# Kernel tuning notes

Measured on AMD Instinct MI355X. Metric: run time of the kernel, lower is better.

The kernel has to match this reference:

```python
import jax, jax.numpy as jnp
import numpy as np

DIM = 384
HEADS = 6
HEAD_DIM = DIM // HEADS
HIDDEN = int(DIM * 4.0)
LS_INIT = 1e-5
EPS = 1e-5


def _ln(x, w, b):
    mu = jnp.mean(x, axis=-1, keepdims=True)
    var = jnp.var(x, axis=-1, keepdims=True)
    return (x - mu) * jax.lax.rsqrt(var + EPS) * w + b


def setup_inputs() -> dict:
    key = jax.random.key(0)
    ks = jax.random.split(key, 12)
    s = 0.02
    eye = jnp.eye(HIDDEN, dtype=jnp.float32)
    return {
        "x": jax.random.normal(ks[0], (8, 2048, DIM), dtype=jnp.float32),
        "qkv_w": jax.random.normal(ks[1], (3 * DIM, DIM), dtype=jnp.float32) * s,
        "qkv_b": jnp.zeros((3 * DIM,), dtype=jnp.float32),
        "proj_w": jax.random.normal(ks[2], (DIM, DIM), dtype=jnp.float32) * s,
        "proj_b": jnp.zeros((DIM,), dtype=jnp.float32),
        "fc1_w": jax.random.normal(ks[3], (HIDDEN, DIM), dtype=jnp.float32) * s,
        "fc1_b": jnp.zeros((HIDDEN,), dtype=jnp.float32),
        "eye1_w": eye + jax.random.normal(ks[4], (HIDDEN, HIDDEN), dtype=jnp.float32) * s,
        "eye2_w": eye + jax.random.normal(ks[5], (HIDDEN, HIDDEN), dtype=jnp.float32) * s,
        "fc2_w": jax.random.normal(ks[6], (DIM, HIDDEN), dtype=jnp.float32) * s,
        "fc2_b": jnp.zeros((DIM,), dtype=jnp.float32),
        "norm1_w": jnp.ones((DIM,), dtype=jnp.float32),
        "norm1_b": jnp.zeros((DIM,), dtype=jnp.float32),
        "norm2_w": jnp.ones((DIM,), dtype=jnp.float32),
        "norm2_b": jnp.zeros((DIM,), dtype=jnp.float32),
        "ls1_gamma": jnp.full((DIM,), LS_INIT, dtype=jnp.float32),
        "ls2_gamma": jnp.full((DIM,), LS_INIT, dtype=jnp.float32),
    }


def reference(x, qkv_w, qkv_b, proj_w, proj_b, fc1_w, fc1_b, eye1_w, eye2_w,
              fc2_w, fc2_b, norm1_w, norm1_b, norm2_w, norm2_b, ls1_gamma, ls2_gamma):
    B, N, C = x.shape
    scale = HEAD_DIM ** -0.5

    # ---- attention branch ----
    h = _ln(x, norm1_w, norm1_b)
    qkv = h @ qkv_w.T + qkv_b                      # [B,N,3C]
    qkv = qkv.reshape(B, N, 3, HEADS, HEAD_DIM)
    q = qkv[:, :, 0].transpose(0, 2, 1, 3) * scale  # [B,H,N,D]
    k = qkv[:, :, 1].transpose(0, 2, 1, 3)
    v = qkv[:, :, 2].transpose(0, 2, 1, 3)
    attn = jax.nn.softmax(jnp.einsum('bhnd,bhmd->bhnm', q, k), axis=-1)  # [B,H,N,N]
    o = jnp.einsum('bhnm,bhmd->bhnd', attn, v)
    o = o.transpose(0, 2, 1, 3).reshape(B, N, C)
    o = o @ proj_w.T + proj_b
    x = x + o * ls1_gamma

    # ---- extended MLP branch (timm Mlp norm is Identity) ----
    h2 = _ln(x, norm2_w, norm2_b)
    a = jax.nn.gelu(h2 @ fc1_w.T + fc1_b, approximate=False)
    a = (a @ eye1_w.T) @ eye2_w.T
    a = a @ fc2_w.T + fc2_b
    return x + a * ls2_gamma
```

## Files before the change

### kernel.cpp

```cpp
#include <hip/hip_runtime.h>
#include <math.h>

#define DIM 384
#define HEADS 6
#define HEAD_DIM 64
#define HIDDEN 1536
#define BATCH 8
#define SEQ 2048
#define TOKENS (BATCH * SEQ)

typedef __bf16 bf16;
typedef float f32x4 __attribute__((ext_vector_type(4)));
typedef float f32x16 __attribute__((ext_vector_type(16)));
typedef int i32x2 __attribute__((ext_vector_type(2)));
typedef int i32x4 __attribute__((ext_vector_type(4)));
typedef int i32x8 __attribute__((ext_vector_type(8)));

#define GLOAD_LDS(gp, lp)                                                      \
    __builtin_amdgcn_global_load_lds(                                          \
        (const __attribute__((address_space(1))) void*)(gp),                   \
        (__attribute__((address_space(3))) void*)(lp), 16, 0, 0)

__device__ __forceinline__ unsigned char to_fp8(float v) {
    return (unsigned char)(__builtin_amdgcn_cvt_pk_fp8_f32(v, v, 0, false) & 0xff);
}

__device__ __forceinline__ i32x8 pack8(i32x4 lo, i32x4 hi) {
    i32x8 r;
#pragma unroll
    for (int j = 0; j < 4; j++) { r[j] = lo[j]; r[4 + j] = hi[j]; }
    return r;
}

#define NW_QKV  (1152 * 384)
#define NW_PROJ (384 * 384)
#define NW_FC1  (1536 * 384)
#define NW_EYE  (1536 * 1536)
#define NW_FC2  (384 * 1536)
#define NW_ALL2 (NW_QKV + NW_PROJ + NW_FC1 + NW_EYE + NW_FC2)

__global__ void convert_w8(const float* __restrict__ qkv, const float* __restrict__ proj,
                           const float* __restrict__ fc1, const float* __restrict__ e2,
                           const float* __restrict__ fc2, unsigned char* __restrict__ dst) {
    int q4 = blockIdx.x * 256 + threadIdx.x;
    int stride = gridDim.x * 256;
    for (; q4 < NW_ALL2 / 4; q4 += stride) {
        int i = q4 * 4;
        int j = i;
        const float* src;
        if (j < NW_QKV) src = qkv;
        else if ((j -= NW_QKV) < NW_PROJ) src = proj;
        else if ((j -= NW_PROJ) < NW_FC1) src = fc1;
        else if ((j -= NW_FC1) < NW_EYE) src = e2;
        else { j -= NW_EYE; src = fc2; }
        float4 v = *(const float4*)(src + j);
        int p = __builtin_amdgcn_cvt_pk_fp8_f32(v.x, v.y, 0, false);
        p = __builtin_amdgcn_cvt_pk_fp8_f32(v.z, v.w, p, true);
        *(int*)(dst + i) = p;
    }
}

__global__ __launch_bounds__(256) void transpose_f8(const float* __restrict__ in,
                                                    unsigned char* __restrict__ outT) {
    __shared__ float t[64][65];
    int r0 = blockIdx.y * 64, c0 = blockIdx.x * 64;
    int tc = threadIdx.x & 63, tr = threadIdx.x >> 6;
#pragma unroll
    for (int i = 0; i < 16; i++) {
        int r = tr + 4 * i;
        t[r][tc] = in[(size_t)(r0 + r) * 1536 + c0 + tc];
    }
    __syncthreads();
    int on = threadIdx.x >> 2;
    int ok0 = (threadIdx.x & 3) * 16;
    i32x4 pk;
#pragma unroll
    for (int q = 0; q < 4; q++) {
        int p = __builtin_amdgcn_cvt_pk_fp8_f32(t[ok0 + 4 * q + 0][on],
                                                t[ok0 + 4 * q + 1][on], 0, false);
        p = __builtin_amdgcn_cvt_pk_fp8_f32(t[ok0 + 4 * q + 2][on],
                                            t[ok0 + 4 * q + 3][on], p, true);
        pk[q] = p;
    }
    *(i32x4*)(outT + (size_t)(c0 + on) * 1536 + r0 + ok0) = pk;
}

__global__ __launch_bounds__(256) void ln_kernel(const float* __restrict__ x,
                                                 const float* __restrict__ w,
                                                 const float* __restrict__ b,
                                                 unsigned char* __restrict__ out) {
    int wave = threadIdx.x >> 6;
    int lane = threadIdx.x & 63;
    int t = blockIdx.x * 4 + wave;
    const float* xr = x + (size_t)t * DIM;
    float v[6];
    float s = 0.f;
#pragma unroll
    for (int i = 0; i < 6; i++) { v[i] = xr[lane + 64 * i]; s += v[i]; }
#pragma unroll
    for (int m = 1; m < 64; m <<= 1) s += __shfl_xor(s, m, 64);
    float mu = s * (1.f / DIM);
    float q = 0.f;
#pragma unroll
    for (int i = 0; i < 6; i++) { float d = v[i] - mu; q += d * d; }
#pragma unroll
    for (int m = 1; m < 64; m <<= 1) q += __shfl_xor(q, m, 64);
    float rstd = rsqrtf(q * (1.f / DIM) + 1e-5f);
    unsigned char* orow = out + (size_t)t * DIM;
#pragma unroll
    for (int i = 0; i < 6; i++) {
        int c = lane + 64 * i;
        orow[c] = to_fp8((v[i] - mu) * rstd * w[c] + b[c]);
    }
}

template <int EPI>
__global__ __launch_bounds__(256) void gemm_f8(const unsigned char* __restrict__ A,
                                               const unsigned char* __restrict__ W,
                                               const float* __restrict__ bias,
                                               float* __restrict__ outf,
                                               const float* __restrict__ resid,
                                               const float* __restrict__ gamma,
                                               unsigned char* __restrict__ vtb8,
                                               unsigned char* __restrict__ out8,
                                               int N, int K) {
    __shared__ __attribute__((aligned(16))) unsigned char As[128 * 128];
    __shared__ __attribute__((aligned(16))) unsigned char Bs[128 * 128];
    int tid = threadIdx.x;
    int wave = tid >> 6, lane = tid & 63;
    int l15 = lane & 15, quad = lane >> 4;
    int bm = blockIdx.y * 128, bn = blockIdx.x * 128;
    int wm = (wave & 1) * 64, wn = (wave >> 1) * 64;
    f32x4 acc[4][4] = {};

    for (int k0 = 0; k0 < K; k0 += 128) {
#pragma unroll
        for (int i = 0; i < 4; i++) {
            int slot = i * 256 + tid;
            int rr = slot >> 3;
            int gg = (slot & 7) ^ (rr & 7);
            GLOAD_LDS(A + (size_t)(bm + rr) * K + k0 + gg * 16,
                      (char*)As + (i * 256 + wave * 64) * 16);
            GLOAD_LDS(W + (size_t)(bn + rr) * K + k0 + gg * 16,
                      (char*)Bs + (i * 256 + wave * 64) * 16);
        }
        __syncthreads();
        i32x8 af[4], bfr[4];
#pragma unroll
        for (int mt = 0; mt < 4; mt++) {
            int rA = wm + mt * 16 + l15;
            const i32x4* p = (const i32x4*)(As + 128 * rA);
            af[mt] = pack8(p[(2 * quad) ^ (rA & 7)], p[(2 * quad + 1) ^ (rA & 7)]);
        }
#pragma unroll
        for (int nt = 0; nt < 4; nt++) {
            int rB = wn + nt * 16 + l15;
            const i32x4* p = (const i32x4*)(Bs + 128 * rB);
            bfr[nt] = pack8(p[(2 * quad) ^ (rB & 7)], p[(2 * quad + 1) ^ (rB & 7)]);
        }
#pragma unroll
        for (int mt = 0; mt < 4; mt++)
#pragma unroll
            for (int nt = 0; nt < 4; nt++)
                acc[mt][nt] = __builtin_amdgcn_mfma_scale_f32_16x16x128_f8f6f4(
                    af[mt], bfr[nt], acc[mt][nt], 0, 0,
                    0, 0x7f7f7f7f, 0, 0x7f7f7f7f);
        __syncthreads();
    }

#pragma unroll
    for (int mt = 0; mt < 4; mt++) {
#pragma unroll
        for (int nt = 0; nt < 4; nt++) {
            int col = bn + wn + nt * 16 + l15;
            int row0 = bm + wm + mt * 16 + quad * 4;
            float v[4];
#pragma unroll
            for (int r = 0; r < 4; r++) {
                v[r] = acc[mt][nt][r];
                if (EPI >= 2) v[r] += bias[col];
                if (EPI == 2) v[r] = 0.5f * v[r] * (1.f + erff(v[r] * 0.70710678118654752f));
            }
            if (EPI == 3) {
#pragma unroll
                for (int r = 0; r < 4; r++) {
                    size_t idx = (size_t)(row0 + r) * N + col;
                    outf[idx] = resid[idx] + v[r] * gamma[col];
                }
            } else if (EPI == 4) {
                if (col < 768) {
                    float sc = (col < 384) ? 0.180336880f : 1.f;
#pragma unroll
                    for (int r = 0; r < 4; r++)
                        out8[(size_t)(row0 + r) * 768 + col] = to_fp8(v[r] * sc);
                } else {
                    int hd = col - 768;
                    int b = row0 >> 11;
                    int n0 = row0 & 2047;
                    int p = __builtin_amdgcn_cvt_pk_fp8_f32(v[0], v[1], 0, false);
                    p = __builtin_amdgcn_cvt_pk_fp8_f32(v[2], v[3], p, true);
                    *(int*)(vtb8 + ((size_t)(b * 384 + hd) << 11) + n0) = p;
                }
            } else {
#pragma unroll
                for (int r = 0; r < 4; r++)
                    out8[(size_t)(row0 + r) * N + col] = to_fp8(v[r]);
            }
        }
    }
}

__global__ __launch_bounds__(256) void gemm_proj_ln(const unsigned char* __restrict__ A,
                                                    const unsigned char* __restrict__ W,
                                                    const float* __restrict__ bias,
                                                    const float* __restrict__ resid,
                                                    const float* __restrict__ gamma,
                                                    const float* __restrict__ n2w,
                                                    const float* __restrict__ n2b,
                                                    float* __restrict__ x1,
                                                    unsigned char* __restrict__ hbuf8) {
    __shared__ __attribute__((aligned(16))) unsigned char As[64 * 128];
    __shared__ __attribute__((aligned(16))) unsigned char Bs[384 * 128];
    int tid = threadIdx.x;
    int wave = tid >> 6, lane = tid & 63;
    int l15 = lane & 15, quad = lane >> 4;
    int bm = blockIdx.x * 64;
    int wm = wave * 16;
    f32x4 acc[24];
#pragma unroll
    for (int i = 0; i < 24; i++) acc[i] = (f32x4){0.f, 0.f, 0.f, 0.f};

    const int K = 384;
    for (int k0 = 0; k0 < K; k0 += 128) {
#pragma unroll
        for (int i = 0; i < 2; i++) {
            int slot = i * 256 + tid;
            int rr = slot >> 3, gg = (slot & 7) ^ (rr & 7);
            GLOAD_LDS(A + (size_t)(bm + rr) * K + k0 + gg * 16, (char*)As + slot * 16);
        }
#pragma unroll
        for (int i = 0; i < 12; i++) {
            int slot = i * 256 + tid;
            int rr = slot >> 3, gg = (slot & 7) ^ (rr & 7);
            GLOAD_LDS(W + (size_t)rr * K + k0 + gg * 16, (char*)Bs + slot * 16);
        }
        __syncthreads();
        int rA = wm + l15;
        const i32x4* pa = (const i32x4*)(As + 128 * rA);
        i32x8 af = pack8(pa[(2 * quad) ^ (rA & 7)], pa[(2 * quad + 1) ^ (rA & 7)]);
#pragma unroll
        for (int nt = 0; nt < 24; nt++) {
            int rB = nt * 16 + l15;
            const i32x4* pb = (const i32x4*)(Bs + 128 * rB);
            i32x8 bf = pack8(pb[(2 * quad) ^ (rB & 7)], pb[(2 * quad + 1) ^ (rB & 7)]);
            acc[nt] = __builtin_amdgcn_mfma_scale_f32_16x16x128_f8f6f4(
                af, bf, acc[nt], 0, 0, 0, 0x7f7f7f7f, 0, 0x7f7f7f7f);
        }
        __syncthreads();
    }

    int row0 = bm + wm + quad * 4;
#pragma unroll
    for (int nt = 0; nt < 24; nt++) {
        int col = nt * 16 + l15;
        float bi = bias[col], ga = gamma[col];
#pragma unroll
        for (int r = 0; r < 4; r++) {
            size_t idx = (size_t)(row0 + r) * DIM + col;
            float v = resid[idx] + (acc[nt][r] + bi) * ga;
            x1[idx] = v;
            acc[nt][r] = v;
        }
    }
#pragma unroll
    for (int r = 0; r < 4; r++) {
        float s = 0.f;
#pragma unroll
        for (int nt = 0; nt < 24; nt++) s += acc[nt][r];
#pragma unroll
        for (int m = 1; m < 16; m <<= 1) s += __shfl_xor(s, m, 64);
        float mu = s * (1.f / DIM);
        float q = 0.f;
#pragma unroll
        for (int nt = 0; nt < 24; nt++) { float d = acc[nt][r] - mu; q += d * d; }
#pragma unroll
        for (int m = 1; m < 16; m <<= 1) q += __shfl_xor(q, m, 64);
        float rstd = rsqrtf(q * (1.f / DIM) + 1e-5f);
        unsigned char* orow = hbuf8 + (size_t)(row0 + r) * DIM;
#pragma unroll
        for (int nt = 0; nt < 24; nt++) {
            int col = nt * 16 + l15;
            orow[col] = to_fp8((acc[nt][r] - mu) * rstd * n2w[col] + n2b[col]);
        }
    }
}

__global__ __launch_bounds__(256, 3) void attn_kernel(const unsigned char* __restrict__ qk8,
                                                      const unsigned char* __restrict__ vtb8,
                                                      unsigned char* __restrict__ o) {
    __shared__ __attribute__((aligned(16))) unsigned char Ks[2][64 * 64];
    __shared__ __attribute__((aligned(16))) unsigned char Vts[2][64 * 64];
    int tid = threadIdx.x, wave = tid >> 6, lane = tid & 63;
    int l31 = lane & 31, h = lane >> 5;
    int bh = blockIdx.y;
    int b = bh / HEADS, hh = bh - b * HEADS;
    int qr0 = blockIdx.x * 128 + wave * 32;
    const unsigned char* base = qk8 + (size_t)b * SEQ * 768;
    const unsigned char* vbase = vtb8 + ((size_t)bh << 17);

    int rr = tid >> 2, ss = tid & 3;
    int fs = (rr >> 1) & 3;
    const unsigned char* kg = base + (size_t)rr * 768 + 384 + hh * 64 + 16 * (ss ^ fs);
    const unsigned char* vg = vbase + ((size_t)rr << 11) + 16 * (ss ^ fs);
    int ldsoff = tid * 16;

    i32x8 aq = *(const i32x8*)(base + (size_t)(qr0 + l31) * 768 + hh * 64 + 32 * h);

    f32x16 oa0 = {}, oa1 = {};
    float lsum = 0.f;
    int swr = (l31 >> 1) & 3;

    GLOAD_LDS(kg, (char*)Ks[0] + ldsoff);
    GLOAD_LDS(vg, (char*)Vts[0] + ldsoff);
    __syncthreads();

    for (int kt = 0; kt < SEQ / 64; kt++) {
        const unsigned char* Kc = Ks[kt & 1];
        const unsigned char* Vc = Vts[kt & 1];
        if (kt + 1 < SEQ / 64) {
            GLOAD_LDS(kg + (size_t)(kt + 1) * 64 * 768, (char*)Ks[(kt + 1) & 1] + ldsoff);
            GLOAD_LDS(vg + (kt + 1) * 64, (char*)Vts[(kt + 1) & 1] + ldsoff);
        }

        int pk[2][4];
#pragma unroll
        for (int mi = 0; mi < 2; mi++) {
            int rK = 32 * mi + l31;
            const i32x4* kp = (const i32x4*)(Kc + rK * 64);
            i32x8 ak = pack8(kp[(2 * h + 0) ^ swr], kp[(2 * h + 1) ^ swr]);
            f32x16 s = {};
            __builtin_amdgcn_s_setprio(1);
            s = __builtin_amdgcn_mfma_scale_f32_32x32x64_f8f6f4(
                ak, aq, s, 0, 0, 0, 0x7f7f7f7f, 0, 0x7f7f7f7f);
            __builtin_amdgcn_s_setprio(0);
#pragma unroll
            for (int g = 0; g < 4; g++) {
                float p0 = __builtin_amdgcn_exp2f(s[4 * g + 0]);
                float p1 = __builtin_amdgcn_exp2f(s[4 * g + 1]);
                float p2 = __builtin_amdgcn_exp2f(s[4 * g + 2]);
                float p3 = __builtin_amdgcn_exp2f(s[4 * g + 3]);
                lsum += (p0 + p1) + (p2 + p3);
                int pkv = __builtin_amdgcn_cvt_pk_fp8_f32(p0, p1, 0, false);
                pkv = __builtin_amdgcn_cvt_pk_fp8_f32(p2, p3, pkv, true);
                pk[mi][g] = pkv;
            }
        }

        i32x8 ap;
#pragma unroll
        for (int g = 0; g < 4; g++) {
            i32x2 r = __builtin_amdgcn_permlane32_swap(pk[0][g], pk[1][g], false, false);
            ap[2 * g] = r[0];
            ap[2 * g + 1] = r[1];
        }

        {
            const i32x4* vp0 = (const i32x4*)(Vc + l31 * 64);
            i32x8 bv0 = pack8(vp0[(2 * h + 0) ^ swr], vp0[(2 * h + 1) ^ swr]);
            const i32x4* vp1 = (const i32x4*)(Vc + (32 + l31) * 64);
            i32x8 bv1 = pack8(vp1[(2 * h + 0) ^ swr], vp1[(2 * h + 1) ^ swr]);
            __builtin_amdgcn_s_setprio(1);
            oa0 = __builtin_amdgcn_mfma_scale_f32_32x32x64_f8f6f4(
                ap, bv0, oa0, 0, 0, 0, 0x7f7f7f7f, 0, 0x7f7f7f7f);
            oa1 = __builtin_amdgcn_mfma_scale_f32_32x32x64_f8f6f4(
                ap, bv1, oa1, 0, 0, 0, 0x7f7f7f7f, 0, 0x7f7f7f7f);
            __builtin_amdgcn_s_setprio(0);
        }
        __syncthreads();
    }

    lsum += __shfl_xor(lsum, 32, 64);

#pragma unroll
    for (int g = 0; g < 4; g++) {
#pragma unroll
        for (int r4 = 0; r4 < 4; r4++) {
            int qloc = r4 + 8 * g + 4 * h;
            float inv = 1.f / __shfl(lsum, qloc, 64);
            int r = 4 * g + r4;
            unsigned char* orow = o + ((size_t)(b * SEQ + qr0 + qloc)) * DIM + hh * 64;
            orow[l31]      = to_fp8(oa0[r] * inv);
            orow[32 + l31] = to_fp8(oa1[r] * inv);
        }
    }
}

extern "C" void kernel_launch(void* const* d_in, const int* in_sizes, int n_in,
                              void* d_out, int out_size, void* d_ws, size_t ws_size,
                              hipStream_t stream) {
    const float* x      = (const float*)d_in[0];
    const float* qkv_w  = (const float*)d_in[1];
    const float* qkv_b  = (const float*)d_in[2];
    const float* proj_w = (const float*)d_in[3];
    const float* proj_b = (const float*)d_in[4];
    const float* fc1_w  = (const float*)d_in[5];
    const float* fc1_b  = (const float*)d_in[6];
    const float* eye1_w = (const float*)d_in[7];
    const float* eye2_w = (const float*)d_in[8];
    const float* fc2_w  = (const float*)d_in[9];
    const float* fc2_b  = (const float*)d_in[10];
    const float* n1w    = (const float*)d_in[11];
    const float* n1b    = (const float*)d_in[12];
    const float* n2w    = (const float*)d_in[13];
    const float* n2b    = (const float*)d_in[14];
    const float* ls1    = (const float*)d_in[15];
    const float* ls2    = (const float*)d_in[16];
    float* out = (float*)d_out;

    char* w = (char*)d_ws;
    size_t off = 0;
    unsigned char* w8 = (unsigned char*)(w + off); off += (size_t)NW_ALL2;
    unsigned char* wqkv8  = w8;
    unsigned char* wproj8 = wqkv8 + NW_QKV;
    unsigned char* wfc18  = wproj8 + NW_PROJ;
    unsigned char* weye28 = wfc18 + NW_FC1;
    unsigned char* wfc28  = weye28 + NW_EYE;
    unsigned char* e1t8  = (unsigned char*)(w + off); off += (size_t)NW_EYE;
    unsigned char* m1t8  = (unsigned char*)(w + off); off += (size_t)NW_EYE;
    unsigned char* wc8   = (unsigned char*)(w + off); off += (size_t)NW_FC2;
    unsigned char* hbuf8 = (unsigned char*)(w + off); off += (size_t)TOKENS * DIM;
    unsigned char* qk8   = (unsigned char*)(w + off); off += (size_t)TOKENS * 768;
    unsigned char* vtb8  = (unsigned char*)(w + off); off += (size_t)TOKENS * DIM;
    unsigned char* obuf8 = (unsigned char*)(w + off); off += (size_t)TOKENS * DIM;
    unsigned char* abuf8 = (unsigned char*)(w + off); off += (size_t)TOKENS * HIDDEN;
    float* x1   = (float*)(w + off); off += (size_t)TOKENS * DIM * 4;

    convert_w8<<<4096, 256, 0, stream>>>(qkv_w, proj_w, fc1_w, eye2_w, fc2_w, w8);

    transpose_f8<<<dim3(24, 24), 256, 0, stream>>>(eye1_w, e1t8);

    gemm_f8<0><<<dim3(1536 / 128, 1536 / 128), 256, 0, stream>>>(
        e1t8, weye28, nullptr, nullptr, nullptr, nullptr, nullptr, m1t8, 1536, 1536);

    gemm_f8<0><<<dim3(1536 / 128, 384 / 128), 256, 0, stream>>>(
        wfc28, m1t8, nullptr, nullptr, nullptr, nullptr, nullptr, wc8, 1536, 1536);

    ln_kernel<<<TOKENS / 4, 256, 0, stream>>>(x, n1w, n1b, hbuf8);

    gemm_f8<4><<<dim3(1152 / 128, TOKENS / 128), 256, 0, stream>>>(
        hbuf8, wqkv8, qkv_b, nullptr, nullptr, nullptr, vtb8, qk8, 1152, 384);

    attn_kernel<<<dim3(SEQ / 128, BATCH * HEADS), 256, 0, stream>>>(qk8, vtb8, obuf8);

    gemm_proj_ln<<<TOKENS / 64, 256, 0, stream>>>(
        obuf8, wproj8, proj_b, x, ls1, n2w, n2b, x1, hbuf8);

    gemm_f8<2><<<dim3(1536 / 128, TOKENS / 128), 256, 0, stream>>>(
        hbuf8, wfc18, fc1_b, nullptr, nullptr, nullptr, nullptr, abuf8, 1536, 384);

    gemm_f8<3><<<dim3(384 / 128, TOKENS / 128), 256, 0, stream>>>(
        abuf8, wc8, fc2_b, out, x1, ls2, nullptr, nullptr, 384, 1536);
}
```

Before: 298.3 us.

## Merge prep kernels into compute launches via block-index dispatch; drop attention setprio

Folds LayerNorm1, the eye1 transpose and the weight fp8 conversion into one heterogeneous launch. The eye1·eye2 GEMM now runs alongside the QKV GEMM in one grid, and the fc2·M1 weight-merge GEMM runs alongside proj+LN2, with block ID selecting the role. This removes four launches and lets the small weight-prep GEMMs fill idle CUs next to the main work. It also drops the s_setprio hints around the attention MFMAs and interleaves the V fragment loads with the MFMAs. Risks: mixed block roles increase shared-memory and register use for every block, which can lower occupancy.

Result: faster. 291.1 us (-2.4%).

```diff
diff --git a/kernel.cpp b/kernel.cpp
--- a/kernel.cpp
+++ b/kernel.cpp
@@ -39,78 +39,98 @@
 #define NW_FC2  (384 * 1536)
 #define NW_ALL2 (NW_QKV + NW_PROJ + NW_FC1 + NW_EYE + NW_FC2)
 
-__global__ void convert_w8(const float* __restrict__ qkv, const float* __restrict__ proj,
-                           const float* __restrict__ fc1, const float* __restrict__ e2,
-                           const float* __restrict__ fc2, unsigned char* __restrict__ dst) {
-    int q4 = blockIdx.x * 256 + threadIdx.x;
-    int stride = gridDim.x * 256;
-    for (; q4 < NW_ALL2 / 4; q4 += stride) {
-        int i = q4 * 4;
-        int j = i;
-        const float* src;
-        if (j < NW_QKV) src = qkv;
-        else if ((j -= NW_QKV) < NW_PROJ) src = proj;
-        else if ((j -= NW_PROJ) < NW_FC1) src = fc1;
-        else if ((j -= NW_FC1) < NW_EYE) src = e2;
-        else { j -= NW_EYE; src = fc2; }
-        float4 v = *(const float4*)(src + j);
-        int p = __builtin_amdgcn_cvt_pk_fp8_f32(v.x, v.y, 0, false);
-        p = __builtin_amdgcn_cvt_pk_fp8_f32(v.z, v.w, p, true);
-        *(int*)(dst + i) = p;
-    }
-}
-
-__global__ __launch_bounds__(256) void transpose_f8(const float* __restrict__ in,
-                                                    unsigned char* __restrict__ outT) {
-    __shared__ float t[64][65];
-    int r0 = blockIdx.y * 64, c0 = blockIdx.x * 64;
-    int tc = threadIdx.x & 63, tr = threadIdx.x >> 6;
-#pragma unroll
-    for (int i = 0; i < 16; i++) {
-        int r = tr + 4 * i;
-        t[r][tc] = in[(size_t)(r0 + r) * 1536 + c0 + tc];
-    }
-    __syncthreads();
-    int on = threadIdx.x >> 2;
-    int ok0 = (threadIdx.x & 3) * 16;
-    i32x4 pk;
-#pragma unroll
-    for (int q = 0; q < 4; q++) {
-        int p = __builtin_amdgcn_cvt_pk_fp8_f32(t[ok0 + 4 * q + 0][on],
-                                                t[ok0 + 4 * q + 1][on], 0, false);
-        p = __builtin_amdgcn_cvt_pk_fp8_f32(t[ok0 + 4 * q + 2][on],
-                                            t[ok0 + 4 * q + 3][on], p, true);
-        pk[q] = p;
-    }
-    *(i32x4*)(outT + (size_t)(c0 + on) * 1536 + r0 + ok0) = pk;
-}
-
-__global__ __launch_bounds__(256) void ln_kernel(const float* __restrict__ x,
-                                                 const float* __restrict__ w,
-                                                 const float* __restrict__ b,
-                                                 unsigned char* __restrict__ out) {
-    int wave = threadIdx.x >> 6;
-    int lane = threadIdx.x & 63;
-    int t = blockIdx.x * 4 + wave;
-    const float* xr = x + (size_t)t * DIM;
-    float v[6];
-    float s = 0.f;
-#pragma unroll
-    for (int i = 0; i < 6; i++) { v[i] = xr[lane + 64 * i]; s += v[i]; }
-#pragma unroll
-    for (int m = 1; m < 64; m <<= 1) s += __shfl_xor(s, m, 64);
-    float mu = s * (1.f / DIM);
-    float q = 0.f;
-#pragma unroll
-    for (int i = 0; i < 6; i++) { float d = v[i] - mu; q += d * d; }
-#pragma unroll
-    for (int m = 1; m < 64; m <<= 1) q += __shfl_xor(q, m, 64);
-    float rstd = rsqrtf(q * (1.f / DIM) + 1e-5f);
-    unsigned char* orow = out + (size_t)t * DIM;
-#pragma unroll
-    for (int i = 0; i < 6; i++) {
-        int c = lane + 64 * i;
-        orow[c] = to_fp8((v[i] - mu) * rstd * w[c] + b[c]);
+template <int EPI>
+__device__ __forceinline__ void gemm_core(const unsigned char* __restrict__ A,
+                                          const unsigned char* __restrict__ W,
+                                          const float* __restrict__ bias,
+                                          float* __restrict__ outf,
+                                          const float* __restrict__ resid,
+                                          const float* __restrict__ gamma,
+                                          unsigned char* __restrict__ vtb8,
+                                          unsigned char* __restrict__ out8,
+                                          int N, int K, int bx, int by,
+                                          unsigned char* As, unsigned char* Bs) {
+    int tid = threadIdx.x;
+    int wave = tid >> 6, lane = tid & 63;
+    int l15 = lane & 15, quad = lane >> 4;
+    int bm = by * 128, bn = bx * 128;
+    int wm = (wave & 1) * 64, wn = (wave >> 1) * 64;
+    f32x4 acc[4][4] = {};
+
+    for (int k0 = 0; k0 < K; k0 += 128) {
+#pragma unroll
+        for (int i = 0; i < 4; i++) {
+            int slot = i * 256 + tid;
+            int rr = slot >> 3;
+            int gg = (slot & 7) ^ (rr & 7);
+            GLOAD_LDS(A + (size_t)(bm + rr) * K + k0 + gg * 16,
+                      (char*)As + (i * 256 + wave * 64) * 16);
+            GLOAD_LDS(W + (size_t)(bn + rr) * K + k0 + gg * 16,
+                      (char*)Bs + (i * 256 + wave * 64) * 16);
+        }
+        __syncthreads();
+        i32x8 af[4], bfr[4];
+#pragma unroll
+        for (int mt = 0; mt < 4; mt++) {
+            int rA = wm + mt * 16 + l15;
+            const i32x4* p = (const i32x4*)(As + 128 * rA);
+            af[mt] = pack8(p[(2 * quad) ^ (rA & 7)], p[(2 * quad + 1) ^ (rA & 7)]);
+        }
+#pragma unroll
+        for (int nt = 0; nt < 4; nt++) {
+            int rB = wn + nt * 16 + l15;
+            const i32x4* p = (const i32x4*)(Bs + 128 * rB);
+            bfr[nt] = pack8(p[(2 * quad) ^ (rB & 7)], p[(2 * quad + 1) ^ (rB & 7)]);
+        }
+#pragma unroll
+        for (int mt = 0; mt < 4; mt++)
+#pragma unroll
+            for (int nt = 0; nt < 4; nt++)
+                acc[mt][nt] = __builtin_amdgcn_mfma_scale_f32_16x16x128_f8f6f4(
+                    af[mt], bfr[nt], acc[mt][nt], 0, 0,
+                    0, 0x7f7f7f7f, 0, 0x7f7f7f7f);
+        __syncthreads();
+    }
+
+#pragma unroll
+    for (int mt = 0; mt < 4; mt++) {
+#pragma unroll
+        for (int nt = 0; nt < 4; nt++) {
+            int col = bn + wn + nt * 16 + l15;
+            int row0 = bm + wm + mt * 16 + quad * 4;
+            float v[4];
+#pragma unroll
+            for (int r = 0; r < 4; r++) {
+                v[r] = acc[mt][nt][r];
+                if (EPI >= 2) v[r] += bias[col];
+                if (EPI == 2) v[r] = 0.5f * v[r] * (1.f + erff(v[r] * 0.70710678118654752f));
+            }
+            if (EPI == 3) {
+#pragma unroll
+                for (int r = 0; r < 4; r++) {
+                    size_t idx = (size_t)(row0 + r) * N + col;
+                    outf[idx] = resid[idx] + v[r] * gamma[col];
+                }
+            } else if (EPI == 4) {
+                if (col < 768) {
+                    float sc = (col < 384) ? 0.180336880f : 1.f;
+#pragma unroll
+                    for (int r = 0; r < 4; r++)
+                        out8[(size_t)(row0 + r) * 768 + col] = to_fp8(v[r] * sc);
+                } else {
+                    int hd = col - 768;
+                    int b = row0 >> 11;
+                    int n0 = row0 & 2047;
+                    int p = __builtin_amdgcn_cvt_pk_fp8_f32(v[0], v[1], 0, false);
+                    p = __builtin_amdgcn_cvt_pk_fp8_f32(v[2], v[3], p, true);
+                    *(int*)(vtb8 + ((size_t)(b * 384 + hd) << 11) + n0) = p;
+                }
+            } else {
+#pragma unroll
+                for (int r = 0; r < 4; r++)
+                    out8[(size_t)(row0 + r) * N + col] = to_fp8(v[r]);
+            }
+        }
     }
 }
 
@@ -126,105 +146,124 @@
                                                int N, int K) {
     __shared__ __attribute__((aligned(16))) unsigned char As[128 * 128];
     __shared__ __attribute__((aligned(16))) unsigned char Bs[128 * 128];
+    gemm_core<EPI>(A, W, bias, outf, resid, gamma, vtb8, out8, N, K,
+                   blockIdx.x, blockIdx.y, As, Bs);
+}
+
+__global__ __launch_bounds__(256) void fused_pre(const float* __restrict__ x,
+                                                 const float* __restrict__ n1w,
+                                                 const float* __restrict__ n1b,
+                                                 unsigned char* __restrict__ hbuf8,
+                                                 const float* __restrict__ e1,
+                                                 unsigned char* __restrict__ e1t8,
+                                                 const float* __restrict__ qkv,
+                                                 const float* __restrict__ proj,
+                                                 const float* __restrict__ fc1,
+                                                 const float* __restrict__ e2,
+                                                 const float* __restrict__ fc2,
+                                                 unsigned char* __restrict__ w8) {
+    __shared__ float tb[64][65];
+    int bid = blockIdx.x;
+    int tid = threadIdx.x;
+    if (bid < 4096) {
+        int wave = tid >> 6, lane = tid & 63;
+        int tok = bid * 4 + wave;
+        const float* xr = x + (size_t)tok * DIM;
+        float v[6];
+        float s = 0.f;
+#pragma unroll
+        for (int i = 0; i < 6; i++) { v[i] = xr[lane + 64 * i]; s += v[i]; }
+#pragma unroll
+        for (int m = 1; m < 64; m <<= 1) s += __shfl_xor(s, m, 64);
+        float mu = s * (1.f / DIM);
+        float q = 0.f;
+#pragma unroll
+        for (int i = 0; i < 6; i++) { float d = v[i] - mu; q += d * d; }
+#pragma unroll
+        for (int m = 1; m < 64; m <<= 1) q += __shfl_xor(q, m, 64);
+        float rstd = rsqrtf(q * (1.f / DIM) + 1e-5f);
+        unsigned char* orow = hbuf8 + (size_t)tok * DIM;
+#pragma unroll
+        for (int i = 0; i < 6; i++) {
+            int c = lane + 64 * i;
+            orow[c] = to_fp8((v[i] - mu) * rstd * n1w[c] + n1b[c]);
+        }
+    } else if (bid < 4096 + 576) {
+        int g = bid - 4096;
+        int r0 = (g / 24) * 64, c0 = (g % 24) * 64;
+        int tc = tid & 63, tr = tid >> 6;
+#pragma unroll
+        for (int i = 0; i < 16; i++) {
+            int r = tr + 4 * i;
+            tb[r][tc] = e1[(size_t)(r0 + r) * 1536 + c0 + tc];
+        }
+        __syncthreads();
+        int on = tid >> 2;
+        int ok0 = (tid & 3) * 16;
+        i32x4 pk;
+#pragma unroll
+        for (int q = 0; q < 4; q++) {
+            int p = __builtin_amdgcn_cvt_pk_fp8_f32(tb[ok0 + 4 * q + 0][on],
+                                                    tb[ok0 + 4 * q + 1][on], 0, false);
+            p = __builtin_amdgcn_cvt_pk_fp8_f32(tb[ok0 + 4 * q + 2][on],
+                                                tb[ok0 + 4 * q + 3][on], p, true);
+            pk[q] = p;
+        }
+        *(i32x4*)(e1t8 + (size_t)(c0 + on) * 1536 + r0 + ok0) = pk;
+    } else {
+        int q4 = (bid - 4672) * 256 + tid;
+        for (; q4 < NW_ALL2 / 4; q4 += 1024 * 256) {
+            int i = q4 * 4;
+            int j = i;
+            const float* src;
+            if (j < NW_QKV) src = qkv;
+            else if ((j -= NW_QKV) < NW_PROJ) src = proj;
+            else if ((j -= NW_PROJ) < NW_FC1) src = fc1;
+            else if ((j -= NW_FC1) < NW_EYE) src = e2;
+            else { j -= NW_EYE; src = fc2; }
+            float4 v = *(const float4*)(src + j);
+            int p = __builtin_amdgcn_cvt_pk_fp8_f32(v.x, v.y, 0, false);
+            p = __builtin_amdgcn_cvt_pk_fp8_f32(v.z, v.w, p, true);
+            *(int*)(w8 + i) = p;
+        }
+    }
+}
+
+__global__ __launch_bounds__(256) void gemm_qkv_prep(const unsigned char* __restrict__ hbuf8,
+                                                     const unsigned char* __restrict__ wqkv8,
+                                                     const float* __restrict__ qkv_b,
+                                                     unsigned char* __restrict__ vtb8,
+                                                     unsigned char* __restrict__ qk8,
+                                                     const unsigned char* __restrict__ e1t8,
+                                                     const unsigned char* __restrict__ weye28,
+                                                     unsigned char* __restrict__ m1t8) {
+    __shared__ __attribute__((aligned(16))) unsigned char As[128 * 128];
+    __shared__ __attribute__((aligned(16))) unsigned char Bs[128 * 128];
+    int bid = blockIdx.x;
+    if (bid < 1152) {
+        gemm_core<4>(hbuf8, wqkv8, qkv_b, nullptr, nullptr, nullptr, vtb8, qk8,
+                     1152, 384, bid % 9, bid / 9, As, Bs);
+    } else {
+        int g = bid - 1152;
+        gemm_core<0>(e1t8, weye28, nullptr, nullptr, nullptr, nullptr, nullptr, m1t8,
+                     1536, 1536, g % 12, g / 12, As, Bs);
+    }
+}
+
+__device__ __forceinline__ void projln_core(const unsigned char* __restrict__ A,
+                                            const unsigned char* __restrict__ W,
+                                            const float* __restrict__ bias,
+                                            const float* __restrict__ resid,
+                                            const float* __restrict__ gamma,
+                                            const float* __restrict__ n2w,
+                                            const float* __restrict__ n2b,
+                                            float* __restrict__ x1,
+                                            unsigned char* __restrict__ hbuf8,
+                                            int bidx, unsigned char* As, unsigned char* Bs) {
     int tid = threadIdx.x;
     int wave = tid >> 6, lane = tid & 63;
     int l15 = lane & 15, quad = lane >> 4;
-    int bm = blockIdx.y * 128, bn = blockIdx.x * 128;
-    int wm = (wave & 1) * 64, wn = (wave >> 1) * 64;
-    f32x4 acc[4][4] = {};
-
-    for (int k0 = 0; k0 < K; k0 += 128) {
-#pragma unroll
-        for (int i = 0; i < 4; i++) {
-            int slot = i * 256 + tid;
-            int rr = slot >> 3;
-            int gg = (slot & 7) ^ (rr & 7);
-            GLOAD_LDS(A + (size_t)(bm + rr) * K + k0 + gg * 16,
-                      (char*)As + (i * 256 + wave * 64) * 16);
-            GLOAD_LDS(W + (size_t)(bn + rr) * K + k0 + gg * 16,
-                      (char*)Bs + (i * 256 + wave * 64) * 16);
-        }
-        __syncthreads();
-        i32x8 af[4], bfr[4];
-#pragma unroll
-        for (int mt = 0; mt < 4; mt++) {
-            int rA = wm + mt * 16 + l15;
-            const i32x4* p = (const i32x4*)(As + 128 * rA);
-            af[mt] = pack8(p[(2 * quad) ^ (rA & 7)], p[(2 * quad + 1) ^ (rA & 7)]);
-        }
-#pragma unroll
-        for (int nt = 0; nt < 4; nt++) {
-            int rB = wn + nt * 16 + l15;
-            const i32x4* p = (const i32x4*)(Bs + 128 * rB);
-            bfr[nt] = pack8(p[(2 * quad) ^ (rB & 7)], p[(2 * quad + 1) ^ (rB & 7)]);
-        }
-#pragma unroll
-        for (int mt = 0; mt < 4; mt++)
-#pragma unroll
-            for (int nt = 0; nt < 4; nt++)
-                acc[mt][nt] = __builtin_amdgcn_mfma_scale_f32_16x16x128_f8f6f4(
-                    af[mt], bfr[nt], acc[mt][nt], 0, 0,
-                    0, 0x7f7f7f7f, 0, 0x7f7f7f7f);
-        __syncthreads();
-    }
-
-#pragma unroll
-    for (int mt = 0; mt < 4; mt++) {
-#pragma unroll
-        for (int nt = 0; nt < 4; nt++) {
-            int col = bn + wn + nt * 16 + l15;
-            int row0 = bm + wm + mt * 16 + quad * 4;
-            float v[4];
-#pragma unroll
-            for (int r = 0; r < 4; r++) {
-                v[r] = acc[mt][nt][r];
-                if (EPI >= 2) v[r] += bias[col];
-                if (EPI == 2) v[r] = 0.5f * v[r] * (1.f + erff(v[r] * 0.70710678118654752f));
-            }
-            if (EPI == 3) {
-#pragma unroll
-                for (int r = 0; r < 4; r++) {
-                    size_t idx = (size_t)(row0 + r) * N + col;
-                    outf[idx] = resid[idx] + v[r] * gamma[col];
-                }
-            } else if (EPI == 4) {
-                if (col < 768) {
-                    float sc = (col < 384) ? 0.180336880f : 1.f;
-#pragma unroll
-                    for (int r = 0; r < 4; r++)
-                        out8[(size_t)(row0 + r) * 768 + col] = to_fp8(v[r] * sc);
-                } else {
-                    int hd = col - 768;
-                    int b = row0 >> 11;
-                    int n0 = row0 & 2047;
-                    int p = __builtin_amdgcn_cvt_pk_fp8_f32(v[0], v[1], 0, false);
-                    p = __builtin_amdgcn_cvt_pk_fp8_f32(v[2], v[3], p, true);
-                    *(int*)(vtb8 + ((size_t)(b * 384 + hd) << 11) + n0) = p;
-                }
-            } else {
-#pragma unroll
-                for (int r = 0; r < 4; r++)
-                    out8[(size_t)(row0 + r) * N + col] = to_fp8(v[r]);
-            }
-        }
-    }
-}
-
-__global__ __launch_bounds__(256) void gemm_proj_ln(const unsigned char* __restrict__ A,
-                                                    const unsigned char* __restrict__ W,
-                                                    const float* __restrict__ bias,
-                                                    const float* __restrict__ resid,
-                                                    const float* __restrict__ gamma,
-                                                    const float* __restrict__ n2w,
-                                                    const float* __restrict__ n2b,
-                                                    float* __restrict__ x1,
-                                                    unsigned char* __restrict__ hbuf8) {
-    __shared__ __attribute__((aligned(16))) unsigned char As[64 * 128];
-    __shared__ __attribute__((aligned(16))) unsigned char Bs[384 * 128];
-    int tid = threadIdx.x;
-    int wave = tid >> 6, lane = tid & 63;
-    int l15 = lane & 15, quad = lane >> 4;
-    int bm = blockIdx.x * 64;
+    int bm = bidx * 64;
     int wm = wave * 16;
     f32x4 acc[24];
 #pragma unroll
@@ -292,6 +331,30 @@
             int col = nt * 16 + l15;
             orow[col] = to_fp8((acc[nt][r] - mu) * rstd * n2w[col] + n2b[col]);
         }
+    }
+}
+
+__global__ __launch_bounds__(256) void gemm_projln_prep(const unsigned char* __restrict__ obuf8,
+                                                        const unsigned char* __restrict__ wproj8,
+                                                        const float* __restrict__ proj_b,
+                                                        const float* __restrict__ x,
+                                                        const float* __restrict__ ls1,
+                                                        const float* __restrict__ n2w,
+                                                        const float* __restrict__ n2b,
+                                                        float* __restrict__ x1,
+                                                        unsigned char* __restrict__ hbuf8,
+                                                        const unsigned char* __restrict__ wfc28,
+                                                        const unsigned char* __restrict__ m1t8,
+                                                        unsigned char* __restrict__ wc8) {
+    __shared__ __attribute__((aligned(16))) unsigned char smem[448 * 128];
+    int bid = blockIdx.x;
+    if (bid < 256) {
+        projln_core(obuf8, wproj8, proj_b, x, ls1, n2w, n2b, x1, hbuf8,
+                    bid, smem, smem + 64 * 128);
+    } else {
+        int g = bid - 256;
+        gemm_core<0>(wfc28, m1t8, nullptr, nullptr, nullptr, nullptr, nullptr, wc8,
+                     1536, 1536, g % 12, g / 12, smem, smem + 128 * 128);
     }
 }
 
@@ -339,10 +402,8 @@
             const i32x4* kp = (const i32x4*)(Kc + rK * 64);
             i32x8 ak = pack8(kp[(2 * h + 0) ^ swr], kp[(2 * h + 1) ^ swr]);
             f32x16 s = {};
-            __builtin_amdgcn_s_setprio(1);
             s = __builtin_amdgcn_mfma_scale_f32_32x32x64_f8f6f4(
                 ak, aq, s, 0, 0, 0, 0x7f7f7f7f, 0, 0x7f7f7f7f);
-            __builtin_amdgcn_s_setprio(0);
 #pragma unroll
             for (int g = 0; g < 4; g++) {
                 float p0 = __builtin_amdgcn_exp2f(s[4 * g + 0]);
@@ -367,14 +428,12 @@
         {
             const i32x4* vp0 = (const i32x4*)(Vc + l31 * 64);
             i32x8 bv0 = pack8(vp0[(2 * h + 0) ^ swr], vp0[(2 * h + 1) ^ swr]);
+            oa0 = __builtin_amdgcn_mfma_scale_f32_32x32x64_f8f6f4(
+                ap, bv0, oa0, 0, 0, 0, 0x7f7f7f7f, 0, 0x7f7f7f7f);
             const i32x4* vp1 = (const i32x4*)(Vc + (32 + l31) * 64);
             i32x8 bv1 = pack8(vp1[(2 * h + 0) ^ swr], vp1[(2 * h + 1) ^ swr]);
-            __builtin_amdgcn_s_setprio(1);
-            oa0 = __builtin_amdgcn_mfma_scale_f32_32x32x64_f8f6f4(
-                ap, bv0, oa0, 0, 0, 0, 0x7f7f7f7f, 0, 0x7f7f7f7f);
             oa1 = __builtin_amdgcn_mfma_scale_f32_32x32x64_f8f6f4(
                 ap, bv1, oa1, 0, 0, 0, 0x7f7f7f7f, 0, 0x7f7f7f7f);
-            __builtin_amdgcn_s_setprio(0);
         }
         __syncthreads();
     }
@@ -435,25 +494,17 @@
     unsigned char* abuf8 = (unsigned char*)(w + off); off += (size_t)TOKENS * HIDDEN;
     float* x1   = (float*)(w + off); off += (size_t)TOKENS * DIM * 4;
 
-    convert_w8<<<4096, 256, 0, stream>>>(qkv_w, proj_w, fc1_w, eye2_w, fc2_w, w8);
-
-    transpose_f8<<<dim3(24, 24), 256, 0, stream>>>(eye1_w, e1t8);
-
-    gemm_f8<0><<<dim3(1536 / 128, 1536 / 128), 256, 0, stream>>>(
-        e1t8, weye28, nullptr, nullptr, nullptr, nullptr, nullptr, m1t8, 1536, 1536);
-
-    gemm_f8<0><<<dim3(1536 / 128, 384 / 128), 256, 0, stream>>>(
-        wfc28, m1t8, nullptr, nullptr, nullptr, nullptr, nullptr, wc8, 1536, 1536);
-
-    ln_kernel<<<TOKENS / 4, 256, 0, stream>>>(x, n1w, n1b, hbuf8);
-
-    gemm_f8<4><<<dim3(1152 / 128, TOKENS / 128), 256, 0, stream>>>(
-        hbuf8, wqkv8, qkv_b, nullptr, nullptr, nullptr, vtb8, qk8, 1152, 384);
+    fused_pre<<<5696, 256, 0, stream>>>(x, n1w, n1b, hbuf8, eye1_w, e1t8,
+                                        qkv_w, proj_w, fc1_w, eye2_w, fc2_w, w8);
+
+    gemm_qkv_prep<<<1152 + 144, 256, 0, stream>>>(hbuf8, wqkv8, qkv_b, vtb8, qk8,
+                                                  e1t8, weye28, m1t8);
 
     attn_kernel<<<dim3(SEQ / 128, BATCH * HEADS), 256, 0, stream>>>(qk8, vtb8, obuf8);
 
-    gemm_proj_ln<<<TOKENS / 64, 256, 0, stream>>>(
-        obuf8, wproj8, proj_b, x, ls1, n2w, n2b, x1, hbuf8);
+    gemm_projln_prep<<<256 + 36, 256, 0, stream>>>(obuf8, wproj8, proj_b, x, ls1,
+                                                   n2w, n2b, x1, hbuf8,
+                                                   wfc28, m1t8, wc8);
 
     gemm_f8<2><<<dim3(1536 / 128, TOKENS / 128), 256, 0, stream>>>(
         hbuf8, wfc18, fc1_b, nullptr, nullptr, nullptr, nullptr, abuf8, 1536, 384);
```
